# Kernel tuning notes

Measured on AMD Instinct MI355X. Metric: run time of the kernel, lower is better.

The kernel has to match this reference:

```python
import jax, jax.numpy as jnp
import numpy as np

B, N, S, K = 8, 16384, 1024, 32
C_STEM, C_PATCH, PE_DIM = 64, 128, 24
RADIUS = 0.2
NUM_BANDS = PE_DIM // 6  # 4 freq bands, sin+cos per xyz axis -> 3*2*4 = 24


def setup_inputs() -> dict:
    key = jax.random.key(0)
    ks = jax.random.split(key, 6)
    xyz = jax.random.uniform(ks[0], (B, N, 3), dtype=jnp.float32)
    point_feature = jax.random.normal(ks[1], (B, N, C_STEM), dtype=jnp.float32)
    patch_center = jax.random.uniform(ks[2], (B, S, 3), dtype=jnp.float32)
    in_dim = C_STEM + 3 + PE_DIM  # grouped_feature + relative_xyz + pos-enc
    w1 = jax.random.normal(ks[3], (in_dim, C_PATCH), dtype=jnp.float32) / np.sqrt(in_dim)
    b1 = jnp.zeros((C_PATCH,), dtype=jnp.float32)
    w2 = jax.random.normal(ks[4], (C_PATCH, C_PATCH), dtype=jnp.float32) / np.sqrt(C_PATCH)
    b2 = jnp.zeros((C_PATCH,), dtype=jnp.float32)
    return dict(xyz=xyz, point_feature=point_feature, patch_center=patch_center,
                w1=w1, b1=b1, w2=w2, b2=b2)


def query_ball_point(radius, nsample, xyz, new_xyz):
    # Standard PointNet++ ball query. xyz:[B,N,3], new_xyz:[B,S,3] -> idx:[B,S,K]
    n = xyz.shape[1]
    sqrdists = jnp.sum((new_xyz[:, :, None, :] - xyz[:, None, :, :]) ** 2, axis=-1)  # [B,S,N]
    gi = jnp.where(sqrdists > radius * radius, n,
                   jnp.arange(n, dtype=jnp.int32)[None, None, :])
    gi = jnp.sort(gi, axis=-1)[:, :, :nsample]           # first K in-ball indices
    first = gi[:, :, :1]
    gi = jnp.where(gi == n, first, gi)                   # pad misses with first hit
    return jnp.minimum(gi, n - 1)


def index_points(points, idx):
    # points:[B,N,C], idx:[B,S,K] -> [B,S,K,C]
    b = points.shape[0]
    return points[jnp.arange(b)[:, None, None], idx]


def pos_encode(rel):
    # NeRF-style sinusoidal encoding of relative xyz: [...,3] -> [...,PE_DIM]
    freqs = (2.0 ** jnp.arange(NUM_BANDS, dtype=jnp.float32)) * jnp.pi
    ang = rel[..., None] * freqs                          # [...,3,NB]
    enc = jnp.concatenate([jnp.sin(ang), jnp.cos(ang)], axis=-1)  # [...,3,2NB]
    return enc.reshape(rel.shape[:-1] + (PE_DIM,))


def reference(xyz, point_feature, patch_center, w1, b1, w2, b2):
    neighbor_idx = query_ball_point(RADIUS, K, xyz, patch_center)   # [B,S,K]
    grouped_xyz = index_points(xyz, neighbor_idx)                    # [B,S,K,3]
    grouped_feature = index_points(point_feature, neighbor_idx)      # [B,S,K,C_STEM]
    relative_xyz = grouped_xyz - patch_center[:, :, None, :]
    relative_position = pos_encode(relative_xyz)                     # [B,S,K,PE_DIM]
    grouped_input = jnp.concatenate(
        (grouped_feature, relative_xyz, relative_position), axis=-1)  # [B,S,K,91]
    h = jax.nn.relu(grouped_input @ w1 + b1)   # PointMLP 1 (shared per-point MLP)
    h = h @ w2 + b2                            # PointMLP 2 (no activation)
    patch_feature = jnp.max(h, axis=2)         # max-pool over K neighbors -> [B,S,C_PATCH]
    return (patch_feature, neighbor_idx)
```

## Files before the change

### kernel.cpp

```cpp
#include <hip/hip_runtime.h>
#include <hip/hip_bf16.h>

#define B_ 8
#define N_ 16384
#define S_ 1024
#define K_ 32
#define CSTEM 64
#define CPATCH 128
#define INDIM 91
#define LDH 136

typedef __attribute__((ext_vector_type(8))) short short8v;
typedef __attribute__((ext_vector_type(4))) float f32x4;

static __device__ __forceinline__ unsigned short f2bf(float f) {
  union { float f; unsigned int u; } v; v.f = f;
  return (unsigned short)((v.u + 0x7FFFu + ((v.u >> 16) & 1u)) >> 16);
}

static __device__ __forceinline__ short8v cvt8(const float4 a, const float4 b) {
  unsigned short v[8];
  v[0] = f2bf(a.x); v[1] = f2bf(a.y); v[2] = f2bf(a.z); v[3] = f2bf(a.w);
  v[4] = f2bf(b.x); v[5] = f2bf(b.y); v[6] = f2bf(b.z); v[7] = f2bf(b.w);
  return *(const short8v*)v;
}

static __device__ __forceinline__ short8v pe_frag(
    float r0, float r1, float r2, int kq)
{
  unsigned short v[8];
  #pragma unroll
  for (int j = 0; j < 8; ++j) {
    const int c = 64 + kq + j;
    float val;
    if (c < 67) {
      val = (c == 64) ? r0 : ((c == 65) ? r1 : r2);
    } else if (c < 91) {
      const int qq = c - 67, d = qq >> 3, rbit = qq & 7, band = rbit & 3;
      const float rel = (d == 0) ? r0 : ((d == 1) ? r1 : r2);
      const float ang = rel * ((float)(1 << band) * 3.14159265358979323846f);
      val = (rbit < 4) ? __sinf(ang) : __cosf(ang);
    } else {
      val = 0.f;
    }
    v[j] = f2bf(val);
  }
  return *(const short8v*)v;
}

__global__ __launch_bounds__(256) void pack_weights(
    const float* __restrict__ w1, const float* __restrict__ w2,
    unsigned short* __restrict__ w1p, unsigned short* __restrict__ w2p)
{
  const int id = blockIdx.x * 256 + threadIdx.x;
  if (id < 3 * 8 * 64) {
    const int l = id & 63, ct = (id >> 6) & 7, ks = id >> 9;
    const int col = 16 * ct + (l & 15);
    const int kb = 32 * ks + (l >> 4) * 8;
    unsigned short v[8];
    #pragma unroll
    for (int j = 0; j < 8; ++j) {
      const int k = kb + j;
      v[j] = (k < INDIM) ? f2bf(w1[k * CPATCH + col]) : (unsigned short)0;
    }
    *(short8v*)&w1p[(size_t)id * 8] = *(const short8v*)v;
  } else if (id < 3 * 8 * 64 + 4 * 8 * 64) {
    const int id2 = id - 3 * 8 * 64;
    const int l = id2 & 63, ct = (id2 >> 6) & 7, ks = id2 >> 9;
    const int col = 16 * ct + (l & 15);
    const int kb = 32 * ks + (l >> 4) * 8;
    unsigned short v[8];
    #pragma unroll
    for (int j = 0; j < 8; ++j) v[j] = f2bf(w2[(kb + j) * CPATCH + col]);
    *(short8v*)&w2p[(size_t)id2 * 8] = *(const short8v*)v;
  }
}

#define FCOMP(V, IDX) (((IDX) & 3) == 0 ? (V)[(IDX) >> 2].x : \
                       ((IDX) & 3) == 1 ? (V)[(IDX) >> 2].y : \
                       ((IDX) & 3) == 2 ? (V)[(IDX) >> 2].z : (V)[(IDX) >> 2].w)

__global__ __launch_bounds__(64, 4) void fused_wave(
    const float* __restrict__ xyz, const float* __restrict__ pf,
    const float* __restrict__ pc,
    const unsigned short* __restrict__ w1p, const float* __restrict__ b1,
    const unsigned short* __restrict__ w2p, const float* __restrict__ b2,
    float* __restrict__ idx_out, float* __restrict__ out)
{
  const int lane = threadIdx.x;
  const int bs   = blockIdx.x;
  const int b    = bs >> 10;

  __shared__ int   sidx[K_];
  __shared__ float sxyz[K_][3];
  __shared__ __align__(16) unsigned short Hs[K_][LDH];

  const float* __restrict__ xb  = xyz + (size_t)b * N_ * 3;
  const float* __restrict__ pfb = pf  + (size_t)b * N_ * CSTEM;
  const float cx = pc[bs * 3 + 0];
  const float cy = pc[bs * 3 + 1];
  const float cz = pc[bs * 3 + 2];
  const double rr = 0.2 * 0.2;

  int found = 0;
  for (int base = 0; base < N_; base += 1024) {
    const int i0 = base + lane * 16;
    float4 v[12];
    #pragma unroll
    for (int t = 0; t < 12; ++t)
      v[t] = *(const float4*)&xb[i0 * 3 + t * 4];

    unsigned mask = 0u;
    #pragma unroll
    for (int p = 0; p < 16; ++p) {
      const float X = FCOMP(v, 3 * p + 0);
      const float Y = FCOMP(v, 3 * p + 1);
      const float Z = FCOMP(v, 3 * p + 2);
      const float dxf = X - cx, dyf = Y - cy, dzf = Z - cz;
      const float d2f = fmaf(dxf, dxf, fmaf(dyf, dyf, dzf * dzf));
      bool in;
      if (fabsf(d2f - 0.04f) <= 1e-5f) {
        const double dx = (double)X - (double)cx;
        const double dy = (double)Y - (double)cy;
        const double dz = (double)Z - (double)cz;
        in = (dx * dx + dy * dy + dz * dz) <= rr;
      } else {
        in = (d2f < 0.04f);
      }
      if (in) mask |= (1u << p);
    }

    const int cnt = __popc(mask);
    int incl = cnt;
    #pragma unroll
    for (int d = 1; d < 64; d <<= 1) {
      const int t = __shfl_up(incl, d);
      if (lane >= d) incl += t;
    }
    const int tot = __shfl(incl, 63);

    int pos = found + (incl - cnt);
    #pragma unroll
    for (int p = 0; p < 16; ++p) {
      if (mask & (1u << p)) {
        if (pos < K_) {
          sidx[pos] = i0 + p;
          sxyz[pos][0] = FCOMP(v, 3 * p + 0);
          sxyz[pos][1] = FCOMP(v, 3 * p + 1);
          sxyz[pos][2] = FCOMP(v, 3 * p + 2);
        }
        ++pos;
      }
    }
    found += tot;
    if (found >= K_) break;
  }

  if (lane == 0 && found == 0) {
    sidx[0] = N_ - 1;
    sxyz[0][0] = xb[(N_ - 1) * 3 + 0];
    sxyz[0][1] = xb[(N_ - 1) * 3 + 1];
    sxyz[0][2] = xb[(N_ - 1) * 3 + 2];
  }
  __threadfence_block();

  if (lane < K_) {
    const int   fill = sidx[0];
    const float fx = sxyz[0][0];
    const float fy = sxyz[0][1];
    const float fz = sxyz[0][2];
    const int v = (lane < found) ? sidx[lane] : fill;
    if (lane >= found) {
      sidx[lane] = fill;
      sxyz[lane][0] = fx;
      sxyz[lane][1] = fy;
      sxyz[lane][2] = fz;
    }
    idx_out[(size_t)bs * K_ + lane] = (float)v;
  }
  __threadfence_block();

  const int rfr  = lane & 15;
  const int koff = (lane >> 4) * 8;

  const int r0 = sidx[rfr];
  const int r1 = sidx[16 + rfr];
  const float4 u00 = *(const float4*)&pfb[(size_t)r0 * CSTEM + koff];
  const float4 u01 = *(const float4*)&pfb[(size_t)r0 * CSTEM + koff + 4];
  const float4 u02 = *(const float4*)&pfb[(size_t)r0 * CSTEM + 32 + koff];
  const float4 u03 = *(const float4*)&pfb[(size_t)r0 * CSTEM + 32 + koff + 4];
  const float4 u10 = *(const float4*)&pfb[(size_t)r1 * CSTEM + koff];
  const float4 u11 = *(const float4*)&pfb[(size_t)r1 * CSTEM + koff + 4];
  const float4 u12 = *(const float4*)&pfb[(size_t)r1 * CSTEM + 32 + koff];
  const float4 u13 = *(const float4*)&pfb[(size_t)r1 * CSTEM + 32 + koff + 4];

  const short8v a0k2 = pe_frag(sxyz[rfr][0] - cx,
                               sxyz[rfr][1] - cy,
                               sxyz[rfr][2] - cz, koff);
  const short8v a1k2 = pe_frag(sxyz[16 + rfr][0] - cx,
                               sxyz[16 + rfr][1] - cy,
                               sxyz[16 + rfr][2] - cz, koff);
  const short8v a0k0 = cvt8(u00, u01), a0k1 = cvt8(u02, u03);
  const short8v a1k0 = cvt8(u10, u11), a1k1 = cvt8(u12, u13);

  #pragma unroll
  for (int c = 0; c < 4; ++c) {
    const short8v bA0 = *(const short8v*)&w1p[((size_t)(0 * 8 + 2 * c + 0) * 64 + lane) * 8];
    const short8v bA1 = *(const short8v*)&w1p[((size_t)(0 * 8 + 2 * c + 1) * 64 + lane) * 8];
    const short8v bB0 = *(const short8v*)&w1p[((size_t)(1 * 8 + 2 * c + 0) * 64 + lane) * 8];
    const short8v bB1 = *(const short8v*)&w1p[((size_t)(1 * 8 + 2 * c + 1) * 64 + lane) * 8];
    const short8v bC0 = *(const short8v*)&w1p[((size_t)(2 * 8 + 2 * c + 0) * 64 + lane) * 8];
    const short8v bC1 = *(const short8v*)&w1p[((size_t)(2 * 8 + 2 * c + 1) * 64 + lane) * 8];

    f32x4 acc[2][2] = {};
    acc[0][0] = __builtin_amdgcn_mfma_f32_16x16x32_bf16(a0k0, bA0, acc[0][0], 0, 0, 0);
    acc[0][1] = __builtin_amdgcn_mfma_f32_16x16x32_bf16(a0k0, bA1, acc[0][1], 0, 0, 0);
    acc[1][0] = __builtin_amdgcn_mfma_f32_16x16x32_bf16(a1k0, bA0, acc[1][0], 0, 0, 0);
    acc[1][1] = __builtin_amdgcn_mfma_f32_16x16x32_bf16(a1k0, bA1, acc[1][1], 0, 0, 0);
    acc[0][0] = __builtin_amdgcn_mfma_f32_16x16x32_bf16(a0k1, bB0, acc[0][0], 0, 0, 0);
    acc[0][1] = __builtin_amdgcn_mfma_f32_16x16x32_bf16(a0k1, bB1, acc[0][1], 0, 0, 0);
    acc[1][0] = __builtin_amdgcn_mfma_f32_16x16x32_bf16(a1k1, bB0, acc[1][0], 0, 0, 0);
    acc[1][1] = __builtin_amdgcn_mfma_f32_16x16x32_bf16(a1k1, bB1, acc[1][1], 0, 0, 0);
    acc[0][0] = __builtin_amdgcn_mfma_f32_16x16x32_bf16(a0k2, bC0, acc[0][0], 0, 0, 0);
    acc[0][1] = __builtin_amdgcn_mfma_f32_16x16x32_bf16(a0k2, bC1, acc[0][1], 0, 0, 0);
    acc[1][0] = __builtin_amdgcn_mfma_f32_16x16x32_bf16(a1k2, bC0, acc[1][0], 0, 0, 0);
    acc[1][1] = __builtin_amdgcn_mfma_f32_16x16x32_bf16(a1k2, bC1, acc[1][1], 0, 0, 0);

    const float bia0 = b1[32 * c + rfr];
    const float bia1 = b1[32 * c + 16 + rfr];
    #pragma unroll
    for (int rt = 0; rt < 2; ++rt)
      #pragma unroll
      for (int reg = 0; reg < 4; ++reg) {
        const int row = 16 * rt + (lane >> 4) * 4 + reg;
        Hs[row][32 * c + rfr]      = f2bf(fmaxf(acc[rt][0][reg] + bia0, 0.f));
        Hs[row][32 * c + 16 + rfr] = f2bf(fmaxf(acc[rt][1][reg] + bia1, 0.f));
      }
  }

  short8v hf[8];
  #pragma unroll
  for (int ks = 0; ks < 4; ++ks) {
    hf[ks * 2 + 0] = *(const short8v*)&Hs[rfr][ks * 32 + koff];
    hf[ks * 2 + 1] = *(const short8v*)&Hs[16 + rfr][ks * 32 + koff];
  }

  #pragma unroll
  for (int c = 0; c < 4; ++c) {
    f32x4 acc2[2][2] = {};
    #pragma unroll
    for (int ks = 0; ks < 4; ++ks) {
      const short8v b0 = *(const short8v*)&w2p[((size_t)(ks * 8 + 2 * c + 0) * 64 + lane) * 8];
      const short8v b1v = *(const short8v*)&w2p[((size_t)(ks * 8 + 2 * c + 1) * 64 + lane) * 8];
      acc2[0][0] = __builtin_amdgcn_mfma_f32_16x16x32_bf16(hf[ks * 2 + 0], b0,  acc2[0][0], 0, 0, 0);
      acc2[0][1] = __builtin_amdgcn_mfma_f32_16x16x32_bf16(hf[ks * 2 + 0], b1v, acc2[0][1], 0, 0, 0);
      acc2[1][0] = __builtin_amdgcn_mfma_f32_16x16x32_bf16(hf[ks * 2 + 1], b0,  acc2[1][0], 0, 0, 0);
      acc2[1][1] = __builtin_amdgcn_mfma_f32_16x16x32_bf16(hf[ks * 2 + 1], b1v, acc2[1][1], 0, 0, 0);
    }
    float m0 = -3.4e38f, m1 = -3.4e38f;
    #pragma unroll
    for (int rt = 0; rt < 2; ++rt)
      #pragma unroll
      for (int reg = 0; reg < 4; ++reg) {
        m0 = fmaxf(m0, acc2[rt][0][reg]);
        m1 = fmaxf(m1, acc2[rt][1][reg]);
      }
    m0 += b2[32 * c + rfr];
    m1 += b2[32 * c + 16 + rfr];
    m0 = fmaxf(m0, __shfl_xor(m0, 16));
    m0 = fmaxf(m0, __shfl_xor(m0, 32));
    m1 = fmaxf(m1, __shfl_xor(m1, 16));
    m1 = fmaxf(m1, __shfl_xor(m1, 32));
    if (lane < 16) {
      out[(size_t)bs * CPATCH + 32 * c + lane]      = m0;
      out[(size_t)bs * CPATCH + 32 * c + 16 + lane] = m1;
    }
  }
}

extern "C" void kernel_launch(void* const* d_in, const int* in_sizes, int n_in,
                              void* d_out, int out_size, void* d_ws, size_t ws_size,
                              hipStream_t stream) {
  const float* xyz = (const float*)d_in[0];
  const float* pf  = (const float*)d_in[1];
  const float* pc  = (const float*)d_in[2];
  const float* w1  = (const float*)d_in[3];
  const float* b1  = (const float*)d_in[4];
  const float* w2  = (const float*)d_in[5];
  const float* b2  = (const float*)d_in[6];

  float* out     = (float*)d_out;
  float* idx_out = out + (size_t)B_ * S_ * CPATCH;

  unsigned short* w1p = (unsigned short*)d_ws;
  unsigned short* w2p = w1p + 96 * 128;

  pack_weights<<<14, 256, 0, stream>>>(w1, w2, w1p, w2p);
  fused_wave<<<B_ * S_, 64, 0, stream>>>(xyz, pf, pc, w1p, b1, w2p, b2,
                                         idx_out, out);
}
```

Measured before the change: 51.57 us.

## Restructure ball-query scan into smaller prefetched chunks with packed dual prefix sum

After: 46.60 us. -9.6%, faster.

```diff
diff --git a/kernel.cpp b/kernel.cpp
--- a/kernel.cpp
+++ b/kernel.cpp
@@ -76,9 +76,42 @@
   }
 }
 
-#define FCOMP(V, IDX) (((IDX) & 3) == 0 ? (V)[(IDX) >> 2].x : \
-                       ((IDX) & 3) == 1 ? (V)[(IDX) >> 2].y : \
-                       ((IDX) & 3) == 2 ? (V)[(IDX) >> 2].z : (V)[(IDX) >> 2].w)
+#define TEST4(V0, V1, V2, MASKVAR) do {                                    \
+    MASKVAR = 0u;                                                          \
+    const float X[4] = {(V0).x, (V0).w, (V1).z, (V2).y};                   \
+    const float Y[4] = {(V0).y, (V1).x, (V1).w, (V2).z};                   \
+    const float Z[4] = {(V0).z, (V1).y, (V2).x, (V2).w};                   \
+    _Pragma("unroll")                                                      \
+    for (int p = 0; p < 4; ++p) {                                          \
+      const float dxf = X[p] - cx, dyf = Y[p] - cy, dzf = Z[p] - cz;       \
+      const float d2f = fmaf(dxf, dxf, fmaf(dyf, dyf, dzf * dzf));         \
+      bool in;                                                             \
+      if (fabsf(d2f - 0.04f) <= 1e-5f) {                                   \
+        const double dx = (double)X[p] - (double)cx;                       \
+        const double dy = (double)Y[p] - (double)cy;                       \
+        const double dz = (double)Z[p] - (double)cz;                       \
+        in = (dx * dx + dy * dy + dz * dz) <= (0.2 * 0.2);                 \
+      } else {                                                             \
+        in = (d2f < 0.04f);                                                \
+      }                                                                    \
+      if (in) MASKVAR |= (1u << p);                                        \
+    }                                                                      \
+  } while (0)
+
+#define APPEND4(MASKVAR, POSVAR, I0, V0, V1, V2) do {                      \
+    if ((MASKVAR) & 1u) { if ((POSVAR) < K_) { sidx[POSVAR] = (I0) + 0;    \
+      sxyz[POSVAR][0] = (V0).x; sxyz[POSVAR][1] = (V0).y;                  \
+      sxyz[POSVAR][2] = (V0).z; } ++(POSVAR); }                            \
+    if ((MASKVAR) & 2u) { if ((POSVAR) < K_) { sidx[POSVAR] = (I0) + 1;    \
+      sxyz[POSVAR][0] = (V0).w; sxyz[POSVAR][1] = (V1).x;                  \
+      sxyz[POSVAR][2] = (V1).y; } ++(POSVAR); }                            \
+    if ((MASKVAR) & 4u) { if ((POSVAR) < K_) { sidx[POSVAR] = (I0) + 2;    \
+      sxyz[POSVAR][0] = (V1).z; sxyz[POSVAR][1] = (V1).w;                  \
+      sxyz[POSVAR][2] = (V2).x; } ++(POSVAR); }                            \
+    if ((MASKVAR) & 8u) { if ((POSVAR) < K_) { sidx[POSVAR] = (I0) + 3;    \
+      sxyz[POSVAR][0] = (V2).y; sxyz[POSVAR][1] = (V2).z;                  \
+      sxyz[POSVAR][2] = (V2).w; } ++(POSVAR); }                            \
+  } while (0)
 
 __global__ __launch_bounds__(64, 4) void fused_wave(
     const float* __restrict__ xyz, const float* __restrict__ pf,
@@ -100,60 +133,53 @@
   const float cx = pc[bs * 3 + 0];
   const float cy = pc[bs * 3 + 1];
   const float cz = pc[bs * 3 + 2];
-  const double rr = 0.2 * 0.2;
 
   int found = 0;
-  for (int base = 0; base < N_; base += 1024) {
-    const int i0 = base + lane * 16;
-    float4 v[12];
-    #pragma unroll
-    for (int t = 0; t < 12; ++t)
-      v[t] = *(const float4*)&xb[i0 * 3 + t * 4];
-
-    unsigned mask = 0u;
-    #pragma unroll
-    for (int p = 0; p < 16; ++p) {
-      const float X = FCOMP(v, 3 * p + 0);
-      const float Y = FCOMP(v, 3 * p + 1);
-      const float Z = FCOMP(v, 3 * p + 2);
-      const float dxf = X - cx, dyf = Y - cy, dzf = Z - cz;
-      const float d2f = fmaf(dxf, dxf, fmaf(dyf, dyf, dzf * dzf));
-      bool in;
-      if (fabsf(d2f - 0.04f) <= 1e-5f) {
-        const double dx = (double)X - (double)cx;
-        const double dy = (double)Y - (double)cy;
-        const double dz = (double)Z - (double)cz;
-        in = (dx * dx + dy * dy + dz * dz) <= rr;
-      } else {
-        in = (d2f < 0.04f);
+  {
+    const int lo3 = lane * 12;
+    int base = 0;
+    float4 v0 = *(const float4*)&xb[lo3 + 0];
+    float4 v1 = *(const float4*)&xb[lo3 + 4];
+    float4 v2 = *(const float4*)&xb[lo3 + 8];
+    float4 v3 = *(const float4*)&xb[256 * 3 + lo3 + 0];
+    float4 v4 = *(const float4*)&xb[256 * 3 + lo3 + 4];
+    float4 v5 = *(const float4*)&xb[256 * 3 + lo3 + 8];
+
+    for (;;) {
+      const int nb = (base + 512 < N_) ? base + 512 : base;
+      const float4 n0 = *(const float4*)&xb[nb * 3 + lo3 + 0];
+      const float4 n1 = *(const float4*)&xb[nb * 3 + lo3 + 4];
+      const float4 n2 = *(const float4*)&xb[nb * 3 + lo3 + 8];
+      const float4 n3 = *(const float4*)&xb[(nb + 256) * 3 + lo3 + 0];
+      const float4 n4 = *(const float4*)&xb[(nb + 256) * 3 + lo3 + 4];
+      const float4 n5 = *(const float4*)&xb[(nb + 256) * 3 + lo3 + 8];
+
+      unsigned m0, m1;
+      TEST4(v0, v1, v2, m0);
+      TEST4(v3, v4, v5, m1);
+
+      const int c0 = __popc(m0), c1 = __popc(m1);
+      unsigned incl = (unsigned)c0 | ((unsigned)c1 << 16);
+      #pragma unroll
+      for (int d = 1; d < 64; d <<= 1) {
+        const unsigned t = (unsigned)__shfl_up((int)incl, d);
+        if (lane >= d) incl += t;
       }
-      if (in) mask |= (1u << p);
-    }
-
-    const int cnt = __popc(mask);
-    int incl = cnt;
-    #pragma unroll
-    for (int d = 1; d < 64; d <<= 1) {
-      const int t = __shfl_up(incl, d);
-      if (lane >= d) incl += t;
-    }
-    const int tot = __shfl(incl, 63);
-
-    int pos = found + (incl - cnt);
-    #pragma unroll
-    for (int p = 0; p < 16; ++p) {
-      if (mask & (1u << p)) {
-        if (pos < K_) {
-          sidx[pos] = i0 + p;
-          sxyz[pos][0] = FCOMP(v, 3 * p + 0);
-          sxyz[pos][1] = FCOMP(v, 3 * p + 1);
-          sxyz[pos][2] = FCOMP(v, 3 * p + 2);
-        }
-        ++pos;
-      }
-    }
-    found += tot;
-    if (found >= K_) break;
+      const unsigned tot = (unsigned)__shfl((int)incl, 63);
+      const int t0 = (int)(tot & 0xFFFFu), t1 = (int)(tot >> 16);
+
+      int pos0 = found + (int)((incl & 0xFFFFu)) - c0;
+      int pos1 = found + t0 + (int)(incl >> 16) - c1;
+      const int i0 = base + lane * 4;
+      APPEND4(m0, pos0, i0, v0, v1, v2);
+      APPEND4(m1, pos1, i0 + 256, v3, v4, v5);
+
+      found += t0 + t1;
+      if (found >= K_) break;
+      base += 512;
+      if (base >= N_) break;
+      v0 = n0; v1 = n1; v2 = n2; v3 = n3; v4 = n4; v5 = n5;
+    }
   }
 
   if (lane == 0 && found == 0) {
```
